# Performance work log

Hardware: AMD Instinct MI355X
Metric: run time of the kernel (lower is better)

The kernel has to match this reference:

```python
import jax, jax.numpy as jnp
import numpy as np


def setup_inputs() -> dict:
    key = jax.random.key(0)
    k1, k2, k3 = jax.random.split(key, 3)
    B, N, K, F, H = 4, 50000, 10, 128, 16
    x = jax.random.normal(k1, (B, N, K, F), dtype=jnp.float32)
    # xavier-like scales for learned params
    W = jax.random.normal(k2, (F, 4 * H), dtype=jnp.float32) * (1.0 / np.sqrt(F))
    a = jax.random.normal(k3, (4, H), dtype=jnp.float32) * 0.5
    return {"x": x, "W": W, "a": a}


def reference(x, W, a):
    # x: [B, N, K, F]; W: [F, 4H] (head-major blocks of 4); a: [4, H]
    B, N, K, F = x.shape
    H = a.shape[1]
    Wr = W.reshape(F, H, 4)                              # per-head projection
    hw = jnp.einsum('bnkf,fhd->bnkhd', x, Wr)            # [B,N,K,H,4]
    logits = jnp.einsum('bnkhd,dh->bnkh', hw, a)         # [B,N,K,H]
    attn = jax.nn.softmax(logits, axis=2)                # softmax over K neighbors
    out = jnp.einsum('bnkh,bnkhd->bnhd', attn, hw)       # [B,N,H,4]
    out = jax.nn.leaky_relu(out, negative_slope=0.2)
    out = out.reshape(B, N, H * 4)                       # concat over heads
    return out.transpose(0, 2, 1)                        # [B, 4H, N]
```

## Files before the change

### kernel.cpp

```cpp
#include <hip/hip_runtime.h>

typedef short bf16x8 __attribute__((ext_vector_type(8)));
typedef float f32x4 __attribute__((ext_vector_type(4)));

constexpr int Bc = 4;
constexpr int Nc = 50000;
constexpr int Kc = 10;
constexpr int Fc = 128;
constexpr int Hc = 16;
constexpr int Cc = 64;
constexpr int NODES = Bc * Nc;
constexpr int NPB = 8;
constexpr int ROWS = NPB * Kc;
constexpr int MT = ROWS / 16;
constexpr int BLK = 256;
constexpr int NTILES = NODES / NPB;

constexpr int LDS_BYTES = 40960;
constexpr int OL_OFF = 21760;

__device__ __forceinline__ unsigned short f2bf(float f) {
    unsigned u = __builtin_bit_cast(unsigned, f);
    return (unsigned short)((u + 0x7fffu + ((u >> 16) & 1u)) >> 16);
}

__device__ __forceinline__ unsigned cvtpk(float lo, float hi) {
    unsigned r;
    asm("v_cvt_pk_bf16_f32 %0, %1, %2" : "=v"(r) : "v"(lo), "v"(hi));
    return r;
}

__global__ __launch_bounds__(256)
void prep_w(const float* __restrict__ W, unsigned short* __restrict__ wt) {
    const int dst = blockIdx.x * 256 + threadIdx.x;
    const int j  = dst & 7;
    const int kc = (dst >> 3) & 3;
    const int l  = (dst >> 5) & 63;
    const int w  = dst >> 11;
    const int c  = w * 16 + (l & 15);
    const int f  = kc * 32 + (l >> 4) * 8 + j;
    wt[dst] = f2bf(W[f * 64 + c]);
}

__global__ __launch_bounds__(BLK, 4)
void gat_kernel(const float* __restrict__ x,
                const unsigned short* __restrict__ wt_ws,
                const float* __restrict__ a,
                float* __restrict__ out)
{
    __shared__ __align__(16) char smem[LDS_BYTES];

    const int t  = threadIdx.x;
    const int w  = t >> 6;
    const int l  = t & 63;
    const int lr = l & 15;
    const int lk = l >> 4;

    bf16x8 bfrag[4];
    {
        const bf16x8* wp = reinterpret_cast<const bf16x8*>(wt_ws + w * 2048 + l * 32);
#pragma unroll
        for (int kc = 0; kc < 4; ++kc) bfrag[kc] = wp[kc];
    }

    {
        const int rsub = w * 2 + (l >> 5);
        const int unit = (l & 31) ^ rsub;
        const char* gsrc = reinterpret_cast<const char*>(x)
                         + (size_t)blockIdx.x * (ROWS * Fc * 4)
                         + rsub * 512 + unit * 16;
#pragma unroll
        for (int j = 0; j < 6; ++j)
            __builtin_amdgcn_global_load_lds(
                (const __attribute__((address_space(1))) void*)(gsrc + j * 4096),
                (__attribute__((address_space(3))) void*)(smem + j * 4096 + w * 1024),
                16, 0, 0);
        __builtin_amdgcn_sched_barrier(0);
#pragma unroll
        for (int j = 6; j < 10; ++j)
            __builtin_amdgcn_global_load_lds(
                (const __attribute__((address_space(1))) void*)(gsrc + j * 4096),
                (__attribute__((address_space(3))) void*)(smem + j * 4096 + w * 1024),
                16, 0, 0);
    }

    f32x4 acc[MT];
#pragma unroll
    for (int m = 0; m < MT; ++m) acc[m] = (f32x4){0.f, 0.f, 0.f, 0.f};

    asm volatile("s_waitcnt vmcnt(4)" ::: "memory");
    __builtin_amdgcn_s_barrier();
    __builtin_amdgcn_sched_barrier(0);

    const int rsw = lr & 7;
#pragma unroll
    for (int m = 0; m < 3; ++m) {
        const char* xrow = smem + (m * 16 + lr) * 512;
#pragma unroll
        for (int kc = 0; kc < 4; ++kc) {
            const int u0 = kc * 8 + lk * 2;
            const f32x4 p0 = *reinterpret_cast<const f32x4*>(xrow + ((u0)     ^ rsw) * 16);
            const f32x4 p1 = *reinterpret_cast<const f32x4*>(xrow + ((u0 + 1) ^ rsw) * 16);
            union { unsigned u[4]; bf16x8 v; } af;
            af.u[0] = cvtpk(p0[0], p0[1]);
            af.u[1] = cvtpk(p0[2], p0[3]);
            af.u[2] = cvtpk(p1[0], p1[1]);
            af.u[3] = cvtpk(p1[2], p1[3]);
            acc[m] = __builtin_amdgcn_mfma_f32_16x16x32_bf16(af.v, bfrag[kc], acc[m], 0, 0, 0);
        }
    }

    asm volatile("s_waitcnt vmcnt(0)" ::: "memory");
    __builtin_amdgcn_s_barrier();
    __builtin_amdgcn_sched_barrier(0);

#pragma unroll
    for (int m = 3; m < MT; ++m) {
        const char* xrow = smem + (m * 16 + lr) * 512;
#pragma unroll
        for (int kc = 0; kc < 4; ++kc) {
            const int u0 = kc * 8 + lk * 2;
            const f32x4 p0 = *reinterpret_cast<const f32x4*>(xrow + ((u0)     ^ rsw) * 16);
            const f32x4 p1 = *reinterpret_cast<const f32x4*>(xrow + ((u0 + 1) ^ rsw) * 16);
            union { unsigned u[4]; bf16x8 v; } af;
            af.u[0] = cvtpk(p0[0], p0[1]);
            af.u[1] = cvtpk(p0[2], p0[3]);
            af.u[2] = cvtpk(p1[0], p1[1]);
            af.u[3] = cvtpk(p1[2], p1[3]);
            acc[m] = __builtin_amdgcn_mfma_f32_16x16x32_bf16(af.v, bfrag[kc], acc[m], 0, 0, 0);
        }
    }

    asm volatile("s_waitcnt lgkmcnt(0)" ::: "memory");
    __builtin_amdgcn_s_barrier();
    __builtin_amdgcn_sched_barrier(0);

    {
        float* hw = reinterpret_cast<float*>(smem);
        const int col = w * 16 + lr;
#pragma unroll
        for (int m = 0; m < MT; ++m) {
            const int rbase = m * 16 + lk * 4;
#pragma unroll
            for (int r = 0; r < 4; ++r)
                hw[(rbase + r) * 68 + col] = acc[m][r];
        }
    }
    __syncthreads();

    if (t < NPB * Hc) {
        const int h  = t & 15;
        const int ln = t >> 4;
        const float ar0 = a[h];
        const float ar1 = a[16 + h];
        const float ar2 = a[32 + h];
        const float ar3 = a[48 + h];
        const float* hwb = reinterpret_cast<const float*>(smem) + (ln * Kc) * 68 + h * 4;

        float mx = -1e30f, lsum = 0.f;
        float o0 = 0.f, o1 = 0.f, o2 = 0.f, o3 = 0.f;
#pragma unroll
        for (int k = 0; k < Kc; ++k) {
            const float4 hv = *reinterpret_cast<const float4*>(hwb + k * 68);
            const float lg = fmaf(hv.x, ar0, fmaf(hv.y, ar1, fmaf(hv.z, ar2, hv.w * ar3)));
            const float mn = fmaxf(mx, lg);
            const float s  = __expf(mx - mn);
            const float p  = __expf(lg - mn);
            mx = mn;
            lsum = fmaf(lsum, s, p);
            o0 = fmaf(o0, s, p * hv.x);
            o1 = fmaf(o1, s, p * hv.y);
            o2 = fmaf(o2, s, p * hv.z);
            o3 = fmaf(o3, s, p * hv.w);
        }
        const float inv = 1.f / lsum;
        o0 *= inv; o1 *= inv; o2 *= inv; o3 *= inv;
        o0 = fmaxf(o0, 0.2f * o0);
        o1 = fmaxf(o1, 0.2f * o1);
        o2 = fmaxf(o2, 0.2f * o2);
        o3 = fmaxf(o3, 0.2f * o3);
        float* ol = reinterpret_cast<float*>(smem + OL_OFF);
        *reinterpret_cast<float4*>(ol + ln * 68 + h * 4) = make_float4(o0, o1, o2, o3);
    }
    __syncthreads();

    if (t < 128) {
        const float* ol = reinterpret_cast<const float*>(smem + OL_OFF);
        const int c  = t >> 1;
        const int nq = t & 1;
        const int nb = blockIdx.x * NPB;
        const int b  = nb / Nc;
        const int n0 = nb - b * Nc;
        float4 v;
        v.x = ol[(nq * 4 + 0) * 68 + c];
        v.y = ol[(nq * 4 + 1) * 68 + c];
        v.z = ol[(nq * 4 + 2) * 68 + c];
        v.w = ol[(nq * 4 + 3) * 68 + c];
        *reinterpret_cast<float4*>(out + ((size_t)b * Cc + c) * Nc + n0 + nq * 4) = v;
    }
}

extern "C" void kernel_launch(void* const* d_in, const int* in_sizes, int n_in,
                              void* d_out, int out_size, void* d_ws, size_t ws_size,
                              hipStream_t stream) {
    const float* x = (const float*)d_in[0];
    const float* W = (const float*)d_in[1];
    const float* a = (const float*)d_in[2];
    float* out = (float*)d_out;
    unsigned short* wt = (unsigned short*)d_ws;

    prep_w<<<32, 256, 0, stream>>>(W, wt);
    gat_kernel<<<NTILES, BLK, 0, stream>>>(x, wt, a, out);
}
```

Measured before the change: 229.1 us.

## Convert to persistent grid with double-buffered LDS prefetch of next tile

Replaces the one-block-per-tile launch with a persistent grid of 512 blocks that stride over tiles. Each block double-buffers the x tile in LDS, issuing global-to-LDS loads for the next tile before computing the current one. The goal is to hide memory latency and cut per-block launch and W/a reload overhead. LDS use per block doubles and occupancy drops to 2 blocks per CU, and 512 blocks may underfill the GPU, which can reduce memory-level parallelism.

New measurement: 244.3 us. 6.6% more time.

```diff
diff --git a/kernel.cpp b/kernel.cpp
--- a/kernel.cpp
+++ b/kernel.cpp
@@ -15,8 +15,10 @@
 constexpr int MT = ROWS / 16;
 constexpr int BLK = 256;
 constexpr int NTILES = NODES / NPB;
-
-constexpr int LDS_BYTES = 40960;
+constexpr int GRID = 512;
+
+constexpr int BUF_BYTES = ROWS * Fc * 4;
+constexpr int LDS_BYTES = 2 * BUF_BYTES;
 constexpr int OL_OFF = 21760;
 
 __device__ __forceinline__ unsigned short f2bf(float f) {
@@ -28,6 +30,13 @@
     unsigned r;
     asm("v_cvt_pk_bf16_f32 %0, %1, %2" : "=v"(r) : "v"(lo), "v"(hi));
     return r;
+}
+
+__device__ __forceinline__ void barrier_lds() {
+    asm volatile("s_waitcnt lgkmcnt(0)" ::: "memory");
+    __builtin_amdgcn_sched_barrier(0);
+    __builtin_amdgcn_s_barrier();
+    __builtin_amdgcn_sched_barrier(0);
 }
 
 __global__ __launch_bounds__(256)
@@ -42,7 +51,7 @@
     wt[dst] = f2bf(W[f * 64 + c]);
 }
 
-__global__ __launch_bounds__(BLK, 4)
+__global__ __launch_bounds__(BLK, 2)
 void gat_kernel(const float* __restrict__ x,
                 const unsigned short* __restrict__ wt_ws,
                 const float* __restrict__ a,
@@ -55,6 +64,7 @@
     const int l  = t & 63;
     const int lr = l & 15;
     const int lk = l >> 4;
+    const int h  = t & 15;
 
     bf16x8 bfrag[4];
     {
@@ -62,141 +72,132 @@
 #pragma unroll
         for (int kc = 0; kc < 4; ++kc) bfrag[kc] = wp[kc];
     }
-
+    const float ar0 = a[h];
+    const float ar1 = a[16 + h];
+    const float ar2 = a[32 + h];
+    const float ar3 = a[48 + h];
+
+    const int rsub = w * 2 + (l >> 5);
+    const int unit = (l & 31) ^ rsub;
+    const size_t lane_goff = (size_t)rsub * 512 + (size_t)unit * 16;
+
+    int tile = blockIdx.x;
     {
-        const int rsub = w * 2 + (l >> 5);
-        const int unit = (l & 31) ^ rsub;
-        const char* gsrc = reinterpret_cast<const char*>(x)
-                         + (size_t)blockIdx.x * (ROWS * Fc * 4)
-                         + rsub * 512 + unit * 16;
-#pragma unroll
-        for (int j = 0; j < 6; ++j)
-            __builtin_amdgcn_global_load_lds(
-                (const __attribute__((address_space(1))) void*)(gsrc + j * 4096),
-                (__attribute__((address_space(3))) void*)(smem + j * 4096 + w * 1024),
-                16, 0, 0);
-        __builtin_amdgcn_sched_barrier(0);
-#pragma unroll
-        for (int j = 6; j < 10; ++j)
+        const char* gsrc = reinterpret_cast<const char*>(x) + (size_t)tile * BUF_BYTES + lane_goff;
+#pragma unroll
+        for (int j = 0; j < 10; ++j)
             __builtin_amdgcn_global_load_lds(
                 (const __attribute__((address_space(1))) void*)(gsrc + j * 4096),
                 (__attribute__((address_space(3))) void*)(smem + j * 4096 + w * 1024),
                 16, 0, 0);
     }
-
-    f32x4 acc[MT];
-#pragma unroll
-    for (int m = 0; m < MT; ++m) acc[m] = (f32x4){0.f, 0.f, 0.f, 0.f};
-
-    asm volatile("s_waitcnt vmcnt(4)" ::: "memory");
-    __builtin_amdgcn_s_barrier();
-    __builtin_amdgcn_sched_barrier(0);
-
-    const int rsw = lr & 7;
-#pragma unroll
-    for (int m = 0; m < 3; ++m) {
-        const char* xrow = smem + (m * 16 + lr) * 512;
-#pragma unroll
-        for (int kc = 0; kc < 4; ++kc) {
-            const int u0 = kc * 8 + lk * 2;
-            const f32x4 p0 = *reinterpret_cast<const f32x4*>(xrow + ((u0)     ^ rsw) * 16);
-            const f32x4 p1 = *reinterpret_cast<const f32x4*>(xrow + ((u0 + 1) ^ rsw) * 16);
-            union { unsigned u[4]; bf16x8 v; } af;
-            af.u[0] = cvtpk(p0[0], p0[1]);
-            af.u[1] = cvtpk(p0[2], p0[3]);
-            af.u[2] = cvtpk(p1[0], p1[1]);
-            af.u[3] = cvtpk(p1[2], p1[3]);
-            acc[m] = __builtin_amdgcn_mfma_f32_16x16x32_bf16(af.v, bfrag[kc], acc[m], 0, 0, 0);
-        }
-    }
-
-    asm volatile("s_waitcnt vmcnt(0)" ::: "memory");
-    __builtin_amdgcn_s_barrier();
-    __builtin_amdgcn_sched_barrier(0);
-
-#pragma unroll
-    for (int m = 3; m < MT; ++m) {
-        const char* xrow = smem + (m * 16 + lr) * 512;
-#pragma unroll
-        for (int kc = 0; kc < 4; ++kc) {
-            const int u0 = kc * 8 + lk * 2;
-            const f32x4 p0 = *reinterpret_cast<const f32x4*>(xrow + ((u0)     ^ rsw) * 16);
-            const f32x4 p1 = *reinterpret_cast<const f32x4*>(xrow + ((u0 + 1) ^ rsw) * 16);
-            union { unsigned u[4]; bf16x8 v; } af;
-            af.u[0] = cvtpk(p0[0], p0[1]);
-            af.u[1] = cvtpk(p0[2], p0[3]);
-            af.u[2] = cvtpk(p1[0], p1[1]);
-            af.u[3] = cvtpk(p1[2], p1[3]);
-            acc[m] = __builtin_amdgcn_mfma_f32_16x16x32_bf16(af.v, bfrag[kc], acc[m], 0, 0, 0);
-        }
-    }
-
-    asm volatile("s_waitcnt lgkmcnt(0)" ::: "memory");
-    __builtin_amdgcn_s_barrier();
-    __builtin_amdgcn_sched_barrier(0);
-
-    {
-        float* hw = reinterpret_cast<float*>(smem);
-        const int col = w * 16 + lr;
+    int p = 0;
+
+    for (;;) {
+        char* Abuf = smem + p * BUF_BYTES;
+        char* Bbuf = smem + (p ^ 1) * BUF_BYTES;
+        const int ntile = tile + GRID;
+
+        if (ntile < NTILES) {
+            const char* gsrc = reinterpret_cast<const char*>(x) + (size_t)ntile * BUF_BYTES + lane_goff;
+#pragma unroll
+            for (int j = 0; j < 10; ++j)
+                __builtin_amdgcn_global_load_lds(
+                    (const __attribute__((address_space(1))) void*)(gsrc + j * 4096),
+                    (__attribute__((address_space(3))) void*)(Bbuf + j * 4096 + w * 1024),
+                    16, 0, 0);
+            asm volatile("s_waitcnt vmcnt(10)" ::: "memory");
+        } else {
+            asm volatile("s_waitcnt vmcnt(0)" ::: "memory");
+        }
+        __builtin_amdgcn_sched_barrier(0);
+        __builtin_amdgcn_s_barrier();
+        __builtin_amdgcn_sched_barrier(0);
+
+        f32x4 acc[MT];
+#pragma unroll
+        for (int m = 0; m < MT; ++m) acc[m] = (f32x4){0.f, 0.f, 0.f, 0.f};
+        const int rsw = lr & 7;
 #pragma unroll
         for (int m = 0; m < MT; ++m) {
-            const int rbase = m * 16 + lk * 4;
-#pragma unroll
-            for (int r = 0; r < 4; ++r)
-                hw[(rbase + r) * 68 + col] = acc[m][r];
-        }
-    }
-    __syncthreads();
-
-    if (t < NPB * Hc) {
-        const int h  = t & 15;
-        const int ln = t >> 4;
-        const float ar0 = a[h];
-        const float ar1 = a[16 + h];
-        const float ar2 = a[32 + h];
-        const float ar3 = a[48 + h];
-        const float* hwb = reinterpret_cast<const float*>(smem) + (ln * Kc) * 68 + h * 4;
-
-        float mx = -1e30f, lsum = 0.f;
-        float o0 = 0.f, o1 = 0.f, o2 = 0.f, o3 = 0.f;
-#pragma unroll
-        for (int k = 0; k < Kc; ++k) {
-            const float4 hv = *reinterpret_cast<const float4*>(hwb + k * 68);
-            const float lg = fmaf(hv.x, ar0, fmaf(hv.y, ar1, fmaf(hv.z, ar2, hv.w * ar3)));
-            const float mn = fmaxf(mx, lg);
-            const float s  = __expf(mx - mn);
-            const float p  = __expf(lg - mn);
-            mx = mn;
-            lsum = fmaf(lsum, s, p);
-            o0 = fmaf(o0, s, p * hv.x);
-            o1 = fmaf(o1, s, p * hv.y);
-            o2 = fmaf(o2, s, p * hv.z);
-            o3 = fmaf(o3, s, p * hv.w);
-        }
-        const float inv = 1.f / lsum;
-        o0 *= inv; o1 *= inv; o2 *= inv; o3 *= inv;
-        o0 = fmaxf(o0, 0.2f * o0);
-        o1 = fmaxf(o1, 0.2f * o1);
-        o2 = fmaxf(o2, 0.2f * o2);
-        o3 = fmaxf(o3, 0.2f * o3);
-        float* ol = reinterpret_cast<float*>(smem + OL_OFF);
-        *reinterpret_cast<float4*>(ol + ln * 68 + h * 4) = make_float4(o0, o1, o2, o3);
-    }
-    __syncthreads();
-
-    if (t < 128) {
-        const float* ol = reinterpret_cast<const float*>(smem + OL_OFF);
-        const int c  = t >> 1;
-        const int nq = t & 1;
-        const int nb = blockIdx.x * NPB;
-        const int b  = nb / Nc;
-        const int n0 = nb - b * Nc;
-        float4 v;
-        v.x = ol[(nq * 4 + 0) * 68 + c];
-        v.y = ol[(nq * 4 + 1) * 68 + c];
-        v.z = ol[(nq * 4 + 2) * 68 + c];
-        v.w = ol[(nq * 4 + 3) * 68 + c];
-        *reinterpret_cast<float4*>(out + ((size_t)b * Cc + c) * Nc + n0 + nq * 4) = v;
+            const char* xrow = Abuf + (m * 16 + lr) * 512;
+#pragma unroll
+            for (int kc = 0; kc < 4; ++kc) {
+                const int u0 = kc * 8 + lk * 2;
+                const f32x4 p0 = *reinterpret_cast<const f32x4*>(xrow + ((u0)     ^ rsw) * 16);
+                const f32x4 p1 = *reinterpret_cast<const f32x4*>(xrow + ((u0 + 1) ^ rsw) * 16);
+                union { unsigned u[4]; bf16x8 v; } af;
+                af.u[0] = cvtpk(p0[0], p0[1]);
+                af.u[1] = cvtpk(p0[2], p0[3]);
+                af.u[2] = cvtpk(p1[0], p1[1]);
+                af.u[3] = cvtpk(p1[2], p1[3]);
+                acc[m] = __builtin_amdgcn_mfma_f32_16x16x32_bf16(af.v, bfrag[kc], acc[m], 0, 0, 0);
+            }
+        }
+        barrier_lds();
+
+        {
+            float* hw = reinterpret_cast<float*>(Abuf);
+            const int col = w * 16 + lr;
+#pragma unroll
+            for (int m = 0; m < MT; ++m) {
+                const int rbase = m * 16 + lk * 4;
+#pragma unroll
+                for (int r = 0; r < 4; ++r)
+                    hw[(rbase + r) * 68 + col] = acc[m][r];
+            }
+        }
+        barrier_lds();
+
+        if (t < NPB * Hc) {
+            const int ln = t >> 4;
+            const float* hwb = reinterpret_cast<const float*>(Abuf) + (ln * Kc) * 68 + h * 4;
+            float mx = -1e30f, lsum = 0.f;
+            float o0 = 0.f, o1 = 0.f, o2 = 0.f, o3 = 0.f;
+#pragma unroll
+            for (int k = 0; k < Kc; ++k) {
+                const float4 hv = *reinterpret_cast<const float4*>(hwb + k * 68);
+                const float lg = fmaf(hv.x, ar0, fmaf(hv.y, ar1, fmaf(hv.z, ar2, hv.w * ar3)));
+                const float mn = fmaxf(mx, lg);
+                const float s  = __expf(mx - mn);
+                const float pp = __expf(lg - mn);
+                mx = mn;
+                lsum = fmaf(lsum, s, pp);
+                o0 = fmaf(o0, s, pp * hv.x);
+                o1 = fmaf(o1, s, pp * hv.y);
+                o2 = fmaf(o2, s, pp * hv.z);
+                o3 = fmaf(o3, s, pp * hv.w);
+            }
+            const float inv = 1.f / lsum;
+            o0 *= inv; o1 *= inv; o2 *= inv; o3 *= inv;
+            o0 = fmaxf(o0, 0.2f * o0);
+            o1 = fmaxf(o1, 0.2f * o1);
+            o2 = fmaxf(o2, 0.2f * o2);
+            o3 = fmaxf(o3, 0.2f * o3);
+            float* ol = reinterpret_cast<float*>(Abuf + OL_OFF);
+            *reinterpret_cast<float4*>(ol + ln * 68 + h * 4) = make_float4(o0, o1, o2, o3);
+        }
+        barrier_lds();
+
+        if (t < 128) {
+            const float* ol = reinterpret_cast<const float*>(Abuf + OL_OFF);
+            const int c  = t >> 1;
+            const int nq = t & 1;
+            const int nb = tile * NPB;
+            const int b  = nb / Nc;
+            const int n0 = nb - b * Nc;
+            float4 v;
+            v.x = ol[(nq * 4 + 0) * 68 + c];
+            v.y = ol[(nq * 4 + 1) * 68 + c];
+            v.z = ol[(nq * 4 + 2) * 68 + c];
+            v.w = ol[(nq * 4 + 3) * 68 + c];
+            *reinterpret_cast<float4*>(out + ((size_t)b * Cc + c) * Nc + n0 + nq * 4) = v;
+        }
+        barrier_lds();
+
+        tile = ntile;
+        p ^= 1;
+        if (tile >= NTILES) break;
     }
 }
 
@@ -210,5 +211,5 @@
     unsigned short* wt = (unsigned short*)d_ws;
 
     prep_w<<<32, 256, 0, stream>>>(W, wt);
-    gat_kernel<<<NTILES, BLK, 0, stream>>>(x, wt, a, out);
-}
+    gat_kernel<<<GRID, BLK, 0, stream>>>(x, wt, a, out);
+}
```

## Split GEMM by row tiles per wave instead of column tiles, drop early block barriers

Applied to the files above, without the earlier changes.

Each wave now owns whole 16-row tiles of x and computes all four 16-column output blocks, holding all 16 B fragments in registers. Previously each wave owned one column block and read every row. Each wave loads and consumes only its own rows, so the pre-compute block barriers go away and x is read from LDS and converted to bf16 once per row instead of four times. In exchange, wave 3 handles two row tiles (an imbalanced tail), register pressure rises, and the LDS buffer shrinks to exactly the x tile.

New measurement: 242.1 us. 1.06x slower.

```diff
diff --git a/kernel.cpp b/kernel.cpp
--- a/kernel.cpp
+++ b/kernel.cpp
@@ -12,11 +12,10 @@
 constexpr int NODES = Bc * Nc;
 constexpr int NPB = 8;
 constexpr int ROWS = NPB * Kc;
-constexpr int MT = ROWS / 16;
 constexpr int BLK = 256;
 constexpr int NTILES = NODES / NPB;
 
-constexpr int LDS_BYTES = 40960;
+constexpr int BUF_BYTES = ROWS * Fc * 4;
 constexpr int OL_OFF = 21760;
 
 __device__ __forceinline__ unsigned short f2bf(float f) {
@@ -28,6 +27,13 @@
     unsigned r;
     asm("v_cvt_pk_bf16_f32 %0, %1, %2" : "=v"(r) : "v"(lo), "v"(hi));
     return r;
+}
+
+__device__ __forceinline__ void barrier_lds() {
+    asm volatile("s_waitcnt lgkmcnt(0)" ::: "memory");
+    __builtin_amdgcn_sched_barrier(0);
+    __builtin_amdgcn_s_barrier();
+    __builtin_amdgcn_sched_barrier(0);
 }
 
 __global__ __launch_bounds__(256)
@@ -36,8 +42,8 @@
     const int j  = dst & 7;
     const int kc = (dst >> 3) & 3;
     const int l  = (dst >> 5) & 63;
-    const int w  = dst >> 11;
-    const int c  = w * 16 + (l & 15);
+    const int n  = dst >> 11;
+    const int c  = n * 16 + (l & 15);
     const int f  = kc * 32 + (l >> 4) * 8 + j;
     wt[dst] = f2bf(W[f * 64 + c]);
 }
@@ -48,105 +54,97 @@
                 const float* __restrict__ a,
                 float* __restrict__ out)
 {
-    __shared__ __align__(16) char smem[LDS_BYTES];
-
-    const int t  = threadIdx.x;
-    const int w  = t >> 6;
-    const int l  = t & 63;
-    const int lr = l & 15;
-    const int lk = l >> 4;
-
-    bf16x8 bfrag[4];
-    {
-        const bf16x8* wp = reinterpret_cast<const bf16x8*>(wt_ws + w * 2048 + l * 32);
-#pragma unroll
-        for (int kc = 0; kc < 4; ++kc) bfrag[kc] = wp[kc];
-    }
-
-    {
-        const int rsub = w * 2 + (l >> 5);
-        const int unit = (l & 31) ^ rsub;
-        const char* gsrc = reinterpret_cast<const char*>(x)
-                         + (size_t)blockIdx.x * (ROWS * Fc * 4)
-                         + rsub * 512 + unit * 16;
-#pragma unroll
-        for (int j = 0; j < 6; ++j)
+    __shared__ __align__(16) char smem[BUF_BYTES];
+
+    const int t   = threadIdx.x;
+    const int w   = t >> 6;
+    const int l   = t & 63;
+    const int lr  = l & 15;
+    const int lk  = l >> 4;
+    const int l5  = l >> 5;
+    const int l31 = l & 31;
+
+    bf16x8 bfrag[4][4];
+#pragma unroll
+    for (int n = 0; n < 4; ++n) {
+        const bf16x8* wp = reinterpret_cast<const bf16x8*>(wt_ws + n * 2048 + l * 32);
+#pragma unroll
+        for (int kc = 0; kc < 4; ++kc) bfrag[n][kc] = wp[kc];
+    }
+    asm volatile("s_waitcnt vmcnt(0)" ::: "memory");
+    __builtin_amdgcn_sched_barrier(0);
+
+    const char* xt = reinterpret_cast<const char*>(x) + (size_t)blockIdx.x * BUF_BYTES;
+
+    auto issue_m = [&](int m) {
+#pragma unroll
+        for (int j = 0; j < 8; ++j) {
+            const int rl   = 2 * j + l5;
+            const int unit = l31 ^ (rl & 7);
             __builtin_amdgcn_global_load_lds(
-                (const __attribute__((address_space(1))) void*)(gsrc + j * 4096),
-                (__attribute__((address_space(3))) void*)(smem + j * 4096 + w * 1024),
+                (const __attribute__((address_space(1))) void*)(xt + (size_t)(m * 16 + rl) * 512 + unit * 16),
+                (__attribute__((address_space(3))) void*)(smem + m * 8192 + j * 1024),
                 16, 0, 0);
-        __builtin_amdgcn_sched_barrier(0);
-#pragma unroll
-        for (int j = 6; j < 10; ++j)
-            __builtin_amdgcn_global_load_lds(
-                (const __attribute__((address_space(1))) void*)(gsrc + j * 4096),
-                (__attribute__((address_space(3))) void*)(smem + j * 4096 + w * 1024),
-                16, 0, 0);
-    }
-
-    f32x4 acc[MT];
-#pragma unroll
-    for (int m = 0; m < MT; ++m) acc[m] = (f32x4){0.f, 0.f, 0.f, 0.f};
-
-    asm volatile("s_waitcnt vmcnt(4)" ::: "memory");
-    __builtin_amdgcn_s_barrier();
-    __builtin_amdgcn_sched_barrier(0);
+        }
+    };
+
+    issue_m(w);
+    if (w == 3) {
+        issue_m(4);
+        asm volatile("s_waitcnt vmcnt(8)" ::: "memory");
+    } else {
+        asm volatile("s_waitcnt vmcnt(0)" ::: "memory");
+    }
+    __builtin_amdgcn_sched_barrier(0);
+
+    f32x4 accA[4], accB[4];
+#pragma unroll
+    for (int n = 0; n < 4; ++n) { accA[n] = (f32x4){0.f,0.f,0.f,0.f}; accB[n] = (f32x4){0.f,0.f,0.f,0.f}; }
 
     const int rsw = lr & 7;
-#pragma unroll
-    for (int m = 0; m < 3; ++m) {
-        const char* xrow = smem + (m * 16 + lr) * 512;
+    auto compute_m = [&](int m, f32x4* acc) {
+        const char* base = smem + m * 8192 + lr * 512;
 #pragma unroll
         for (int kc = 0; kc < 4; ++kc) {
             const int u0 = kc * 8 + lk * 2;
-            const f32x4 p0 = *reinterpret_cast<const f32x4*>(xrow + ((u0)     ^ rsw) * 16);
-            const f32x4 p1 = *reinterpret_cast<const f32x4*>(xrow + ((u0 + 1) ^ rsw) * 16);
+            const f32x4 p0 = *reinterpret_cast<const f32x4*>(base + ((u0)     ^ rsw) * 16);
+            const f32x4 p1 = *reinterpret_cast<const f32x4*>(base + ((u0 + 1) ^ rsw) * 16);
             union { unsigned u[4]; bf16x8 v; } af;
             af.u[0] = cvtpk(p0[0], p0[1]);
             af.u[1] = cvtpk(p0[2], p0[3]);
             af.u[2] = cvtpk(p1[0], p1[1]);
             af.u[3] = cvtpk(p1[2], p1[3]);
-            acc[m] = __builtin_amdgcn_mfma_f32_16x16x32_bf16(af.v, bfrag[kc], acc[m], 0, 0, 0);
-        }
-    }
-
-    asm volatile("s_waitcnt vmcnt(0)" ::: "memory");
-    __builtin_amdgcn_s_barrier();
-    __builtin_amdgcn_sched_barrier(0);
-
-#pragma unroll
-    for (int m = 3; m < MT; ++m) {
-        const char* xrow = smem + (m * 16 + lr) * 512;
-#pragma unroll
-        for (int kc = 0; kc < 4; ++kc) {
-            const int u0 = kc * 8 + lk * 2;
-            const f32x4 p0 = *reinterpret_cast<const f32x4*>(xrow + ((u0)     ^ rsw) * 16);
-            const f32x4 p1 = *reinterpret_cast<const f32x4*>(xrow + ((u0 + 1) ^ rsw) * 16);
-            union { unsigned u[4]; bf16x8 v; } af;
-            af.u[0] = cvtpk(p0[0], p0[1]);
-            af.u[1] = cvtpk(p0[2], p0[3]);
-            af.u[2] = cvtpk(p1[0], p1[1]);
-            af.u[3] = cvtpk(p1[2], p1[3]);
-            acc[m] = __builtin_amdgcn_mfma_f32_16x16x32_bf16(af.v, bfrag[kc], acc[m], 0, 0, 0);
-        }
-    }
-
-    asm volatile("s_waitcnt lgkmcnt(0)" ::: "memory");
-    __builtin_amdgcn_s_barrier();
-    __builtin_amdgcn_sched_barrier(0);
+#pragma unroll
+            for (int n = 0; n < 4; ++n)
+                acc[n] = __builtin_amdgcn_mfma_f32_16x16x32_bf16(af.v, bfrag[n][kc], acc[n], 0, 0, 0);
+        }
+    };
+
+    compute_m(w, accA);
+    if (w == 3) {
+        asm volatile("s_waitcnt vmcnt(0)" ::: "memory");
+        __builtin_amdgcn_sched_barrier(0);
+        compute_m(4, accB);
+    }
+
+    barrier_lds();
 
     {
         float* hw = reinterpret_cast<float*>(smem);
-        const int col = w * 16 + lr;
-#pragma unroll
-        for (int m = 0; m < MT; ++m) {
-            const int rbase = m * 16 + lk * 4;
+#pragma unroll
+        for (int n = 0; n < 4; ++n)
 #pragma unroll
             for (int r = 0; r < 4; ++r)
-                hw[(rbase + r) * 68 + col] = acc[m][r];
-        }
-    }
-    __syncthreads();
+                hw[(w * 16 + lk * 4 + r) * 68 + n * 16 + lr] = accA[n][r];
+        if (w == 3) {
+#pragma unroll
+            for (int n = 0; n < 4; ++n)
+#pragma unroll
+                for (int r = 0; r < 4; ++r)
+                    hw[(4 * 16 + lk * 4 + r) * 68 + n * 16 + lr] = accB[n][r];
+        }
+    }
+    barrier_lds();
 
     if (t < NPB * Hc) {
         const int h  = t & 15;
@@ -182,7 +180,7 @@
         float* ol = reinterpret_cast<float*>(smem + OL_OFF);
         *reinterpret_cast<float4*>(ol + ln * 68 + h * 4) = make_float4(o0, o1, o2, o3);
     }
-    __syncthreads();
+    barrier_lds();
 
     if (t < 128) {
         const float* ol = reinterpret_cast<const float*>(smem + OL_OFF);
```

## Convert GAT kernel to persistent grid with cross-tile prefetch into shared LDS buffer

Applied to the files above, without the earlier changes.

Launches a fixed grid of 1024 persistent blocks that loop over tiles. Half of the next tile's x rows are prefetched into LDS while the current tile's epilogue runs, and the other half after it. LDS use drops to a single 40KB buffer, with the hw/output staging placed in the already-consumed upper region. This aims to hide global-load latency and cut block launch overhead, at the cost of extra barriers per tile and fewer resident blocks overlapping memory traffic.

Result: slower. 257.8 us (+12.5%).

```diff
diff --git a/kernel.cpp b/kernel.cpp
--- a/kernel.cpp
+++ b/kernel.cpp
@@ -15,9 +15,10 @@
 constexpr int MT = ROWS / 16;
 constexpr int BLK = 256;
 constexpr int NTILES = NODES / NPB;
-
-constexpr int LDS_BYTES = 40960;
-constexpr int OL_OFF = 21760;
+constexpr int GRID = 1024;
+
+constexpr int BUF_BYTES = ROWS * Fc * 4;
+constexpr int HW_OFF = 20480;
 
 __device__ __forceinline__ unsigned short f2bf(float f) {
     unsigned u = __builtin_bit_cast(unsigned, f);
@@ -28,6 +29,13 @@
     unsigned r;
     asm("v_cvt_pk_bf16_f32 %0, %1, %2" : "=v"(r) : "v"(lo), "v"(hi));
     return r;
+}
+
+__device__ __forceinline__ void barrier_lds() {
+    asm volatile("s_waitcnt lgkmcnt(0)" ::: "memory");
+    __builtin_amdgcn_sched_barrier(0);
+    __builtin_amdgcn_s_barrier();
+    __builtin_amdgcn_sched_barrier(0);
 }
 
 __global__ __launch_bounds__(256)
@@ -36,8 +44,8 @@
     const int j  = dst & 7;
     const int kc = (dst >> 3) & 3;
     const int l  = (dst >> 5) & 63;
-    const int w  = dst >> 11;
-    const int c  = w * 16 + (l & 15);
+    const int n  = dst >> 11;
+    const int c  = n * 16 + (l & 15);
     const int f  = kc * 32 + (l >> 4) * 8 + j;
     wt[dst] = f2bf(W[f * 64 + c]);
 }
@@ -48,13 +56,16 @@
                 const float* __restrict__ a,
                 float* __restrict__ out)
 {
-    __shared__ __align__(16) char smem[LDS_BYTES];
-
-    const int t  = threadIdx.x;
-    const int w  = t >> 6;
-    const int l  = t & 63;
-    const int lr = l & 15;
-    const int lk = l >> 4;
+    __shared__ __align__(16) char smem[BUF_BYTES];
+
+    const int t   = threadIdx.x;
+    const int w   = t >> 6;
+    const int l   = t & 63;
+    const int lr  = l & 15;
+    const int lk  = l >> 4;
+    const int l5  = l >> 5;
+    const int l31 = l & 31;
+    const int h   = t & 15;
 
     bf16x8 bfrag[4];
     {
@@ -62,141 +73,154 @@
 #pragma unroll
         for (int kc = 0; kc < 4; ++kc) bfrag[kc] = wp[kc];
     }
-
-    {
-        const int rsub = w * 2 + (l >> 5);
-        const int unit = (l & 31) ^ rsub;
-        const char* gsrc = reinterpret_cast<const char*>(x)
-                         + (size_t)blockIdx.x * (ROWS * Fc * 4)
-                         + rsub * 512 + unit * 16;
-#pragma unroll
-        for (int j = 0; j < 6; ++j)
+    const float ar0 = a[h];
+    const float ar1 = a[16 + h];
+    const float ar2 = a[32 + h];
+    const float ar3 = a[48 + h];
+    asm volatile("s_waitcnt vmcnt(0)" ::: "memory");
+    __builtin_amdgcn_sched_barrier(0);
+
+    const int rsub = w * 2 + l5;
+    const int unit = l31 ^ rsub;
+    const size_t lane_goff = (size_t)rsub * 512 + (size_t)unit * 16;
+
+    auto issue = [&](int tl, int j0, int j1) {
+        const char* gsrc = reinterpret_cast<const char*>(x) + (size_t)tl * BUF_BYTES + lane_goff;
+        for (int j = j0; j < j1; ++j)
             __builtin_amdgcn_global_load_lds(
                 (const __attribute__((address_space(1))) void*)(gsrc + j * 4096),
                 (__attribute__((address_space(3))) void*)(smem + j * 4096 + w * 1024),
                 16, 0, 0);
-        __builtin_amdgcn_sched_barrier(0);
-#pragma unroll
-        for (int j = 6; j < 10; ++j)
-            __builtin_amdgcn_global_load_lds(
-                (const __attribute__((address_space(1))) void*)(gsrc + j * 4096),
-                (__attribute__((address_space(3))) void*)(smem + j * 4096 + w * 1024),
-                16, 0, 0);
-    }
-
-    f32x4 acc[MT];
-#pragma unroll
-    for (int m = 0; m < MT; ++m) acc[m] = (f32x4){0.f, 0.f, 0.f, 0.f};
-
-    asm volatile("s_waitcnt vmcnt(4)" ::: "memory");
-    __builtin_amdgcn_s_barrier();
-    __builtin_amdgcn_sched_barrier(0);
+    };
+
+    int tile = blockIdx.x;
+    issue(tile, 0, 5);
+    issue(tile, 5, 10);
 
     const int rsw = lr & 7;
-#pragma unroll
-    for (int m = 0; m < 3; ++m) {
-        const char* xrow = smem + (m * 16 + lr) * 512;
-#pragma unroll
-        for (int kc = 0; kc < 4; ++kc) {
-            const int u0 = kc * 8 + lk * 2;
-            const f32x4 p0 = *reinterpret_cast<const f32x4*>(xrow + ((u0)     ^ rsw) * 16);
-            const f32x4 p1 = *reinterpret_cast<const f32x4*>(xrow + ((u0 + 1) ^ rsw) * 16);
-            union { unsigned u[4]; bf16x8 v; } af;
-            af.u[0] = cvtpk(p0[0], p0[1]);
-            af.u[1] = cvtpk(p0[2], p0[3]);
-            af.u[2] = cvtpk(p1[0], p1[1]);
-            af.u[3] = cvtpk(p1[2], p1[3]);
-            acc[m] = __builtin_amdgcn_mfma_f32_16x16x32_bf16(af.v, bfrag[kc], acc[m], 0, 0, 0);
-        }
-    }
-
-    asm volatile("s_waitcnt vmcnt(0)" ::: "memory");
-    __builtin_amdgcn_s_barrier();
-    __builtin_amdgcn_sched_barrier(0);
-
-#pragma unroll
-    for (int m = 3; m < MT; ++m) {
-        const char* xrow = smem + (m * 16 + lr) * 512;
-#pragma unroll
-        for (int kc = 0; kc < 4; ++kc) {
-            const int u0 = kc * 8 + lk * 2;
-            const f32x4 p0 = *reinterpret_cast<const f32x4*>(xrow + ((u0)     ^ rsw) * 16);
-            const f32x4 p1 = *reinterpret_cast<const f32x4*>(xrow + ((u0 + 1) ^ rsw) * 16);
-            union { unsigned u[4]; bf16x8 v; } af;
-            af.u[0] = cvtpk(p0[0], p0[1]);
-            af.u[1] = cvtpk(p0[2], p0[3]);
-            af.u[2] = cvtpk(p1[0], p1[1]);
-            af.u[3] = cvtpk(p1[2], p1[3]);
-            acc[m] = __builtin_amdgcn_mfma_f32_16x16x32_bf16(af.v, bfrag[kc], acc[m], 0, 0, 0);
-        }
-    }
-
-    asm volatile("s_waitcnt lgkmcnt(0)" ::: "memory");
-    __builtin_amdgcn_s_barrier();
-    __builtin_amdgcn_sched_barrier(0);
-
-    {
-        float* hw = reinterpret_cast<float*>(smem);
-        const int col = w * 16 + lr;
-#pragma unroll
-        for (int m = 0; m < MT; ++m) {
-            const int rbase = m * 16 + lk * 4;
-#pragma unroll
-            for (int r = 0; r < 4; ++r)
-                hw[(rbase + r) * 68 + col] = acc[m][r];
-        }
-    }
-    __syncthreads();
-
-    if (t < NPB * Hc) {
-        const int h  = t & 15;
-        const int ln = t >> 4;
-        const float ar0 = a[h];
-        const float ar1 = a[16 + h];
-        const float ar2 = a[32 + h];
-        const float ar3 = a[48 + h];
-        const float* hwb = reinterpret_cast<const float*>(smem) + (ln * Kc) * 68 + h * 4;
-
-        float mx = -1e30f, lsum = 0.f;
-        float o0 = 0.f, o1 = 0.f, o2 = 0.f, o3 = 0.f;
-#pragma unroll
-        for (int k = 0; k < Kc; ++k) {
-            const float4 hv = *reinterpret_cast<const float4*>(hwb + k * 68);
-            const float lg = fmaf(hv.x, ar0, fmaf(hv.y, ar1, fmaf(hv.z, ar2, hv.w * ar3)));
-            const float mn = fmaxf(mx, lg);
-            const float s  = __expf(mx - mn);
-            const float p  = __expf(lg - mn);
-            mx = mn;
-            lsum = fmaf(lsum, s, p);
-            o0 = fmaf(o0, s, p * hv.x);
-            o1 = fmaf(o1, s, p * hv.y);
-            o2 = fmaf(o2, s, p * hv.z);
-            o3 = fmaf(o3, s, p * hv.w);
-        }
-        const float inv = 1.f / lsum;
-        o0 *= inv; o1 *= inv; o2 *= inv; o3 *= inv;
-        o0 = fmaxf(o0, 0.2f * o0);
-        o1 = fmaxf(o1, 0.2f * o1);
-        o2 = fmaxf(o2, 0.2f * o2);
-        o3 = fmaxf(o3, 0.2f * o3);
-        float* ol = reinterpret_cast<float*>(smem + OL_OFF);
-        *reinterpret_cast<float4*>(ol + ln * 68 + h * 4) = make_float4(o0, o1, o2, o3);
-    }
-    __syncthreads();
-
-    if (t < 128) {
-        const float* ol = reinterpret_cast<const float*>(smem + OL_OFF);
-        const int c  = t >> 1;
-        const int nq = t & 1;
-        const int nb = blockIdx.x * NPB;
-        const int b  = nb / Nc;
-        const int n0 = nb - b * Nc;
-        float4 v;
-        v.x = ol[(nq * 4 + 0) * 68 + c];
-        v.y = ol[(nq * 4 + 1) * 68 + c];
-        v.z = ol[(nq * 4 + 2) * 68 + c];
-        v.w = ol[(nq * 4 + 3) * 68 + c];
-        *reinterpret_cast<float4*>(out + ((size_t)b * Cc + c) * Nc + n0 + nq * 4) = v;
+    for (;;) {
+        const int ntile = tile + GRID;
+
+        asm volatile("s_waitcnt vmcnt(5)" ::: "memory");
+        __builtin_amdgcn_sched_barrier(0);
+        __builtin_amdgcn_s_barrier();
+        __builtin_amdgcn_sched_barrier(0);
+
+        f32x4 acc[MT];
+#pragma unroll
+        for (int m = 0; m < MT; ++m) acc[m] = (f32x4){0.f, 0.f, 0.f, 0.f};
+
+#pragma unroll
+        for (int m = 0; m < 2; ++m) {
+            const char* xrow = smem + (m * 16 + lr) * 512;
+#pragma unroll
+            for (int kc = 0; kc < 4; ++kc) {
+                const int u0 = kc * 8 + lk * 2;
+                const f32x4 p0 = *reinterpret_cast<const f32x4*>(xrow + ((u0)     ^ rsw) * 16);
+                const f32x4 p1 = *reinterpret_cast<const f32x4*>(xrow + ((u0 + 1) ^ rsw) * 16);
+                union { unsigned u[4]; bf16x8 v; } af;
+                af.u[0] = cvtpk(p0[0], p0[1]);
+                af.u[1] = cvtpk(p0[2], p0[3]);
+                af.u[2] = cvtpk(p1[0], p1[1]);
+                af.u[3] = cvtpk(p1[2], p1[3]);
+                acc[m] = __builtin_amdgcn_mfma_f32_16x16x32_bf16(af.v, bfrag[kc], acc[m], 0, 0, 0);
+            }
+        }
+
+        asm volatile("s_waitcnt vmcnt(0)" ::: "memory");
+        __builtin_amdgcn_sched_barrier(0);
+        __builtin_amdgcn_s_barrier();
+        __builtin_amdgcn_sched_barrier(0);
+
+#pragma unroll
+        for (int m = 2; m < MT; ++m) {
+            const char* xrow = smem + (m * 16 + lr) * 512;
+#pragma unroll
+            for (int kc = 0; kc < 4; ++kc) {
+                const int u0 = kc * 8 + lk * 2;
+                const f32x4 p0 = *reinterpret_cast<const f32x4*>(xrow + ((u0)     ^ rsw) * 16);
+                const f32x4 p1 = *reinterpret_cast<const f32x4*>(xrow + ((u0 + 1) ^ rsw) * 16);
+                union { unsigned u[4]; bf16x8 v; } af;
+                af.u[0] = cvtpk(p0[0], p0[1]);
+                af.u[1] = cvtpk(p0[2], p0[3]);
+                af.u[2] = cvtpk(p1[0], p1[1]);
+                af.u[3] = cvtpk(p1[2], p1[3]);
+                acc[m] = __builtin_amdgcn_mfma_f32_16x16x32_bf16(af.v, bfrag[kc], acc[m], 0, 0, 0);
+            }
+        }
+
+        barrier_lds();
+
+        if (ntile < NTILES) issue(ntile, 0, 5);
+
+        {
+            float* hw = reinterpret_cast<float*>(smem + HW_OFF);
+            const int col = w * 16 + lr;
+#pragma unroll
+            for (int m = 0; m < MT; ++m) {
+                const int rbase = m * 16 + lk * 4;
+#pragma unroll
+                for (int r = 0; r < 4; ++r)
+                    hw[(rbase + r) * 64 + col] = acc[m][r];
+            }
+        }
+        barrier_lds();
+
+        float o0, o1, o2, o3;
+        if (t < NPB * Hc) {
+            const int ln = t >> 4;
+            const float* hwb = reinterpret_cast<const float*>(smem + HW_OFF) + (ln * Kc) * 64 + h * 4;
+            float mx = -1e30f, lsum = 0.f;
+            o0 = 0.f; o1 = 0.f; o2 = 0.f; o3 = 0.f;
+#pragma unroll
+            for (int k = 0; k < Kc; ++k) {
+                const float4 hv = *reinterpret_cast<const float4*>(hwb + k * 64);
+                const float lg = fmaf(hv.x, ar0, fmaf(hv.y, ar1, fmaf(hv.z, ar2, hv.w * ar3)));
+                const float mn = fmaxf(mx, lg);
+                const float s  = __expf(mx - mn);
+                const float p  = __expf(lg - mn);
+                mx = mn;
+                lsum = fmaf(lsum, s, p);
+                o0 = fmaf(o0, s, p * hv.x);
+                o1 = fmaf(o1, s, p * hv.y);
+                o2 = fmaf(o2, s, p * hv.z);
+                o3 = fmaf(o3, s, p * hv.w);
+            }
+            const float inv = 1.f / lsum;
+            o0 *= inv; o1 *= inv; o2 *= inv; o3 *= inv;
+            o0 = fmaxf(o0, 0.2f * o0);
+            o1 = fmaxf(o1, 0.2f * o1);
+            o2 = fmaxf(o2, 0.2f * o2);
+            o3 = fmaxf(o3, 0.2f * o3);
+        }
+        barrier_lds();
+
+        if (t < NPB * Hc) {
+            float* ol = reinterpret_cast<float*>(smem + HW_OFF);
+            *reinterpret_cast<float4*>(ol + (t >> 4) * 68 + h * 4) = make_float4(o0, o1, o2, o3);
+        }
+        barrier_lds();
+
+        if (t < 128) {
+            const float* ol = reinterpret_cast<const float*>(smem + HW_OFF);
+            const int c  = t >> 1;
+            const int nq = t & 1;
+            const int nb = tile * NPB;
+            const int b  = nb / Nc;
+            const int n0 = nb - b * Nc;
+            float4 v;
+            v.x = ol[(nq * 4 + 0) * 68 + c];
+            v.y = ol[(nq * 4 + 1) * 68 + c];
+            v.z = ol[(nq * 4 + 2) * 68 + c];
+            v.w = ol[(nq * 4 + 3) * 68 + c];
+            *reinterpret_cast<float4*>(out + ((size_t)b * Cc + c) * Nc + n0 + nq * 4) = v;
+        }
+        barrier_lds();
+
+        if (ntile < NTILES) issue(ntile, 5, 10);
+
+        tile = ntile;
+        if (tile >= NTILES) break;
     }
 }
 
@@ -210,5 +234,5 @@
     unsigned short* wt = (unsigned short*)d_ws;
 
     prep_w<<<32, 256, 0, stream>>>(W, wt);
-    gat_kernel<<<NTILES, BLK, 0, stream>>>(x, wt, a, out);
-}
+    gat_kernel<<<GRID, BLK, 0, stream>>>(x, wt, a, out);
+}
```
